# Kernel tuning notes

Measured on AMD Instinct MI355X. Metric: run time of the kernel, lower is better.

The kernel has to match this reference:

```python
import jax, jax.numpy as jnp
import numpy as np

B, N, E = 2, 4096, 768
H = 12
HD = E // H  # 64

def setup_inputs() -> dict:
    key = jax.random.key(0)
    k1, k2, k3, k4, k5 = jax.random.split(key, 5)
    s = 0.02
    return {
        "x": jax.random.normal(k1, (B, N, E), dtype=jnp.float32),
        "w_qkv": jax.random.normal(k2, (3 * E, E), dtype=jnp.float32) * s,
        "b_qkv": jax.random.normal(k3, (3 * E,), dtype=jnp.float32) * s,
        "w_proj": jax.random.normal(k4, (E, E), dtype=jnp.float32) * s,
        "b_proj": jax.random.normal(k5, (E,), dtype=jnp.float32) * s,
    }

def reference(x, w_qkv, b_qkv, w_proj, b_proj):
    b, n, e = x.shape
    hd = e // H
    # fused QKV projection (torch Linear: x @ W.T + b)
    qkv = jnp.einsum('bne,fe->bnf', x, w_qkv) + b_qkv          # [B,N,3E]
    # faithful to torch reshape(B,N,H,3*hd).permute(0,2,1,3).chunk(3,-1)
    qkv = qkv.reshape(b, n, H, 3 * hd).transpose(0, 2, 1, 3)    # [B,H,N,3hd]
    q, k, v = jnp.split(qkv, 3, axis=-1)                        # each [B,H,N,hd]
    attn = jnp.einsum('bhqd,bhkd->bhqk', q, k) / jnp.sqrt(jnp.float32(hd))
    attn = jax.nn.softmax(attn, axis=-1)                        # [B,H,N,N]
    # dropout layers are identity in eval mode
    out = jnp.einsum('bhqk,bhkd->bhqd', attn, v)                # [B,H,N,hd]
    out = out.transpose(0, 2, 1, 3).reshape(b, n, e)            # [B,N,E]
    out = jnp.einsum('bne,fe->bnf', out, w_proj) + b_proj
    return out
```

## Files before the change

### kernel.cpp

```cpp
#include <hip/hip_runtime.h>

typedef unsigned short u16;
typedef __bf16 bf16x8 __attribute__((ext_vector_type(8)));
typedef float f32x4 __attribute__((ext_vector_type(4)));
typedef unsigned short u16x8 __attribute__((ext_vector_type(8)));
typedef unsigned short u16x4 __attribute__((ext_vector_type(4)));

__device__ __forceinline__ u16 f2bf(float f) {
    __bf16 h = (__bf16)f;
    union { __bf16 h; u16 u; } cv; cv.h = h;
    return cv.u;
}

__device__ __forceinline__ f32x4 mfma16(bf16x8 a, bf16x8 b, f32x4 c) {
    return __builtin_amdgcn_mfma_f32_16x16x32_bf16(a, b, c, 0, 0, 0);
}

__device__ __forceinline__ void gll16(const u16* gp, u16* lp) {
    __builtin_amdgcn_global_load_lds(
        (__attribute__((address_space(1))) void*)const_cast<u16*>(gp),
        (__attribute__((address_space(3))) void*)lp,
        16, 0, 0);
}

__global__ __launch_bounds__(256) void cvt_bf16(const float* __restrict__ in,
                                                u16* __restrict__ out) {
    int i = blockIdx.x * 256 + threadIdx.x;
    const float4* p = (const float4*)in;
    float4 a = p[2 * i];
    float4 b = p[2 * i + 1];
    u16x8 r;
    r[0] = f2bf(a.x); r[1] = f2bf(a.y); r[2] = f2bf(a.z); r[3] = f2bf(a.w);
    r[4] = f2bf(b.x); r[5] = f2bf(b.y); r[6] = f2bf(b.z); r[7] = f2bf(b.w);
    *(u16x8*)&out[8 * i] = r;
}

__global__ __launch_bounds__(256) void gemm_qkv(
    const u16* __restrict__ A, const u16* __restrict__ W,
    const float* __restrict__ bias,
    u16* __restrict__ Qg, u16* __restrict__ Kg, u16* __restrict__ Vtg)
{
    __shared__ __attribute__((aligned(16))) u16 As[128 * 32];
    __shared__ __attribute__((aligned(16))) u16 Bs[128 * 32];
    const int tid = threadIdx.x;
    const int lane = tid & 63, wave = tid >> 6;
    const int lo = lane & 15, hi = lane >> 4;
    const int wm = (wave >> 1) * 64, wn = (wave & 1) * 64;
    const int m0 = blockIdx.y * 128, n0 = blockIdx.x * 128;

    f32x4 acc[4][4];
#pragma unroll
    for (int i = 0; i < 4; i++)
#pragma unroll
        for (int j = 0; j < 4; j++) acc[i][j] = f32x4{0.f, 0.f, 0.f, 0.f};

    const int ar = tid >> 2, ac = (tid & 3) * 8;
    const u16* ga = A + (size_t)(m0 + ar) * 768 + ac;
    const u16* gb = W + (size_t)(n0 + ar) * 768 + ac;

    for (int kt = 0; kt < 768; kt += 32) {
        gll16(ga + kt,            &As[tid * 8]);
        gll16(ga + kt + 64 * 768, &As[2048 + tid * 8]);
        gll16(gb + kt,            &Bs[tid * 8]);
        gll16(gb + kt + 64 * 768, &Bs[2048 + tid * 8]);
        __syncthreads();
        bf16x8 af[4], bfr[4];
#pragma unroll
        for (int mi = 0; mi < 4; mi++)
            af[mi] = *(const bf16x8*)&As[(wm + mi * 16 + lo) * 32 + hi * 8];
#pragma unroll
        for (int ni = 0; ni < 4; ni++)
            bfr[ni] = *(const bf16x8*)&Bs[(wn + ni * 16 + lo) * 32 + hi * 8];
#pragma unroll
        for (int mi = 0; mi < 4; mi++)
#pragma unroll
            for (int ni = 0; ni < 4; ni++)
                acc[mi][ni] = mfma16(af[mi], bfr[ni], acc[mi][ni]);
        __syncthreads();
    }

#pragma unroll
    for (int ni = 0; ni < 4; ni++) {
        const int n = n0 + wn + ni * 16 + lo;
        const int h = n / 192;
        const int rem = n - h * 192;
        const int sel = rem >> 6;
        const int d = rem & 63;
        const float bv = bias[n];
#pragma unroll
        for (int mi = 0; mi < 4; mi++) {
#pragma unroll
            for (int r = 0; r < 4; r++) {
                const int m = m0 + wm + mi * 16 + hi * 4 + r;
                const int bb = m >> 12;
                const int q = m & 4095;
                const float v = acc[mi][ni][r] + bv;
                const size_t bh = (size_t)(bb * 12 + h);
                if (sel == 0) {
                    Qg[(bh * 4096 + q) * 64 + d] = f2bf(v * 0.18033688011112042f);
                } else if (sel == 1) {
                    Kg[(bh * 4096 + q) * 64 + (d ^ ((q & 7) * 8))] = f2bf(v);
                } else {
                    Vtg[(bh * 64 + d) * 4096 +
                        ((q & ~63) | ((q & 63) ^ ((d & 7) * 8)))] = f2bf(v);
                }
            }
        }
    }
}

__global__ __launch_bounds__(256, 3) void attn_kernel(
    const u16* __restrict__ Qg, const u16* __restrict__ Kg,
    const u16* __restrict__ Vtg, u16* __restrict__ Ob)
{
    __shared__ __attribute__((aligned(16))) u16 Ks[128 * 64];
    __shared__ __attribute__((aligned(16))) u16 Vt[64 * 128];
    __shared__ __attribute__((aligned(16))) u16 Ps[8][16 * 64];
    const int tid = threadIdx.x;
    const int lane = tid & 63, wave = tid >> 6;
    const int lo = lane & 15, hi = lane >> 4;
    const int qt = blockIdx.x, h = blockIdx.y, b = blockIdx.z;
    const size_t bh = (size_t)(b * 12 + h);
    const int swl = (lo & 7) * 8;

    bf16x8 qf[2][2];
#pragma unroll
    for (int t = 0; t < 2; t++) {
        const int qrow = qt * 128 + wave * 32 + t * 16 + lo;
        const u16* qp = Qg + (bh * 4096 + qrow) * 64 + hi * 8;
        qf[t][0] = *(const bf16x8*)qp;
        qf[t][1] = *(const bf16x8*)(qp + 32);
    }
    f32x4 o[2][4];
#pragma unroll
    for (int t = 0; t < 2; t++)
#pragma unroll
        for (int i = 0; i < 4; i++) o[t][i] = f32x4{0.f, 0.f, 0.f, 0.f};
    float lp[2] = {0.f, 0.f};

    const u16* gk = Kg + (bh * 4096 + (tid >> 3)) * 64 + (tid & 7) * 8;
    const u16* gv = Vtg + (bh * 64 + (tid >> 4)) * 4096 + (tid & 15) * 8;

    for (int kt = 0; kt < 4096; kt += 128) {
#pragma unroll
        for (int c = 0; c < 4; c++)
            gll16(gk + (size_t)(kt + c * 32) * 64, &Ks[c * 2048 + tid * 8]);
#pragma unroll
        for (int c = 0; c < 4; c++)
            gll16(gv + kt + (size_t)c * 16 * 4096, &Vt[c * 2048 + tid * 8]);
        __syncthreads();

#pragma unroll
        for (int half = 0; half < 2; half++) {
            f32x4 st[2][4];
#pragma unroll
            for (int ni = 0; ni < 4; ni++) {
                const int row = half * 64 + ni * 16 + lo;
                const bf16x8 kf0 = *(const bf16x8*)&Ks[row * 64 + ((hi * 8) ^ swl)];
                const bf16x8 kf1 = *(const bf16x8*)&Ks[row * 64 + ((32 + hi * 8) ^ swl)];
                st[0][ni] = mfma16(kf0, qf[0][0], f32x4{0.f, 0.f, 0.f, 0.f});
                st[0][ni] = mfma16(kf1, qf[0][1], st[0][ni]);
                st[1][ni] = mfma16(kf0, qf[1][0], f32x4{0.f, 0.f, 0.f, 0.f});
                st[1][ni] = mfma16(kf1, qf[1][1], st[1][ni]);
            }
#pragma unroll
            for (int t = 0; t < 2; t++) {
#pragma unroll
                for (int ni = 0; ni < 4; ni++) {
                    u16x4 w;
#pragma unroll
                    for (int r = 0; r < 4; r++) {
                        const float p = __builtin_amdgcn_exp2f(st[t][ni][r]);
                        lp[t] += p;
                        w[r] = f2bf(p);
                    }
                    *(u16x4*)&Ps[wave * 2 + t]
                        [lo * 64 + ((ni * 16 + hi * 4) ^ swl)] = w;
                }
            }
            bf16x8 pf[2][2];
#pragma unroll
            for (int t = 0; t < 2; t++)
#pragma unroll
                for (int p = 0; p < 2; p++)
                    pf[t][p] = *(const bf16x8*)&Ps[wave * 2 + t]
                        [lo * 64 + ((p * 32 + hi * 8) ^ swl)];

#pragma unroll
            for (int di = 0; di < 4; di++) {
                const int base = (di * 16 + lo) * 128 + half * 64;
#pragma unroll
                for (int p = 0; p < 2; p++) {
                    const bf16x8 vt = *(const bf16x8*)
                        &Vt[base + ((p * 32 + hi * 8) ^ swl)];
                    o[0][di] = mfma16(pf[0][p], vt, o[0][di]);
                    o[1][di] = mfma16(pf[1][p], vt, o[1][di]);
                }
            }
        }
        __syncthreads();
    }

#pragma unroll
    for (int t = 0; t < 2; t++) {
        lp[t] += __shfl_xor(lp[t], 16, 64);
        lp[t] += __shfl_xor(lp[t], 32, 64);
    }

#pragma unroll
    for (int t = 0; t < 2; t++) {
#pragma unroll
        for (int r = 0; r < 4; r++) {
            const float rs = __shfl(lp[t], hi * 4 + r, 64);
            const float inv = 1.f / rs;
            const int q = qt * 128 + wave * 32 + t * 16 + hi * 4 + r;
            u16* op = Ob + ((size_t)b * 4096 + q) * 768 + h * 64 + lo;
#pragma unroll
            for (int di = 0; di < 4; di++)
                op[di * 16] = f2bf(o[t][di][r] * inv);
        }
    }
}

__global__ __launch_bounds__(256) void gemm_proj(
    const u16* __restrict__ A, const u16* __restrict__ W,
    const float* __restrict__ bias, float* __restrict__ C)
{
    __shared__ __attribute__((aligned(16))) u16 As[128 * 32];
    __shared__ __attribute__((aligned(16))) u16 Bs[128 * 32];
    const int tid = threadIdx.x;
    const int lane = tid & 63, wave = tid >> 6;
    const int lo = lane & 15, hi = lane >> 4;
    const int wm = (wave >> 1) * 64, wn = (wave & 1) * 64;
    const int m0 = blockIdx.y * 128, n0 = blockIdx.x * 128;

    f32x4 acc[4][4];
#pragma unroll
    for (int i = 0; i < 4; i++)
#pragma unroll
        for (int j = 0; j < 4; j++) acc[i][j] = f32x4{0.f, 0.f, 0.f, 0.f};

    const int ar = tid >> 2, ac = (tid & 3) * 8;
    const u16* ga = A + (size_t)(m0 + ar) * 768 + ac;
    const u16* gb = W + (size_t)(n0 + ar) * 768 + ac;

    for (int kt = 0; kt < 768; kt += 32) {
        gll16(ga + kt,            &As[tid * 8]);
        gll16(ga + kt + 64 * 768, &As[2048 + tid * 8]);
        gll16(gb + kt,            &Bs[tid * 8]);
        gll16(gb + kt + 64 * 768, &Bs[2048 + tid * 8]);
        __syncthreads();
        bf16x8 af[4], bfr[4];
#pragma unroll
        for (int mi = 0; mi < 4; mi++)
            af[mi] = *(const bf16x8*)&As[(wm + mi * 16 + lo) * 32 + hi * 8];
#pragma unroll
        for (int ni = 0; ni < 4; ni++)
            bfr[ni] = *(const bf16x8*)&Bs[(wn + ni * 16 + lo) * 32 + hi * 8];
#pragma unroll
        for (int mi = 0; mi < 4; mi++)
#pragma unroll
            for (int ni = 0; ni < 4; ni++)
                acc[mi][ni] = mfma16(af[mi], bfr[ni], acc[mi][ni]);
        __syncthreads();
    }

#pragma unroll
    for (int ni = 0; ni < 4; ni++) {
        const int n = n0 + wn + ni * 16 + lo;
        const float bv = bias[n];
#pragma unroll
        for (int mi = 0; mi < 4; mi++) {
#pragma unroll
            for (int r = 0; r < 4; r++) {
                const int m = m0 + wm + mi * 16 + hi * 4 + r;
                C[(size_t)m * 768 + n] = acc[mi][ni][r] + bv;
            }
        }
    }
}

extern "C" void kernel_launch(void* const* d_in, const int* in_sizes, int n_in,
                              void* d_out, int out_size, void* d_ws, size_t ws_size,
                              hipStream_t stream)
{
    const float* x      = (const float*)d_in[0];
    const float* w_qkv  = (const float*)d_in[1];
    const float* b_qkv  = (const float*)d_in[2];
    const float* w_proj = (const float*)d_in[3];
    const float* b_proj = (const float*)d_in[4];
    float* out = (float*)d_out;

    u16* ws  = (u16*)d_ws;
    u16* xb  = ws;
    u16* wqb = xb + 6291456;
    u16* wpb = wqb + 1769472;
    u16* Qg  = wpb + 589824;
    u16* Kg  = Qg + 6291456;
    u16* Vtg = Kg + 6291456;
    u16* Ob  = Vtg + 6291456;

    cvt_bf16<<<3072, 256, 0, stream>>>(x, xb);
    cvt_bf16<<<864,  256, 0, stream>>>(w_qkv, wqb);
    cvt_bf16<<<288,  256, 0, stream>>>(w_proj, wpb);
    gemm_qkv<<<dim3(18, 64), 256, 0, stream>>>(xb, wqb, b_qkv, Qg, Kg, Vtg);
    attn_kernel<<<dim3(32, 12, 2), 256, 0, stream>>>(Qg, Kg, Vtg, Ob);
    gemm_proj<<<dim3(6, 64), 256, 0, stream>>>(Ob, wpb, b_proj, out);
}
```

Baseline: 324.9 us.

## Use single-wave attention blocks loading K/V directly into registers

Attention is restructured so each block is one wave handling 64 query rows. K and V^T tiles are loaded straight from global memory into registers, with no LDS staging and no block barriers, and the swizzled K/V layouts written by the QKV GEMM are removed. The three conversion kernels are also merged into one launch to cut launch overhead. The risk is that K/V reuse across waves through LDS is lost, so global and L2 traffic rises. Register pressure also grows with four query tiles per wave.

```diff
diff --git a/kernel.cpp b/kernel.cpp
--- a/kernel.cpp
+++ b/kernel.cpp
@@ -23,16 +23,24 @@
         16, 0, 0);
 }
 
-__global__ __launch_bounds__(256) void cvt_bf16(const float* __restrict__ in,
-                                                u16* __restrict__ out) {
-    int i = blockIdx.x * 256 + threadIdx.x;
-    const float4* p = (const float4*)in;
+__global__ __launch_bounds__(256) void cvt_all(
+    const float* __restrict__ x, const float* __restrict__ wq,
+    const float* __restrict__ wp,
+    u16* __restrict__ xb, u16* __restrict__ wqb, u16* __restrict__ wpb)
+{
+    const int blk = blockIdx.x;
+    const float* src; u16* dst; int base;
+    if (blk < 3072)      { src = x;  dst = xb;  base = 0; }
+    else if (blk < 3936) { src = wq; dst = wqb; base = 3072; }
+    else                 { src = wp; dst = wpb; base = 3936; }
+    const int i = (blk - base) * 256 + threadIdx.x;
+    const float4* p = (const float4*)src;
     float4 a = p[2 * i];
     float4 b = p[2 * i + 1];
     u16x8 r;
     r[0] = f2bf(a.x); r[1] = f2bf(a.y); r[2] = f2bf(a.z); r[3] = f2bf(a.w);
     r[4] = f2bf(b.x); r[5] = f2bf(b.y); r[6] = f2bf(b.z); r[7] = f2bf(b.w);
-    *(u16x8*)&out[8 * i] = r;
+    *(u16x8*)&dst[8 * i] = r;
 }
 
 __global__ __launch_bounds__(256) void gemm_qkv(
@@ -99,121 +107,104 @@
                 if (sel == 0) {
                     Qg[(bh * 4096 + q) * 64 + d] = f2bf(v * 0.18033688011112042f);
                 } else if (sel == 1) {
-                    Kg[(bh * 4096 + q) * 64 + (d ^ ((q & 7) * 8))] = f2bf(v);
+                    Kg[(bh * 4096 + q) * 64 + d] = f2bf(v);
                 } else {
-                    Vtg[(bh * 64 + d) * 4096 +
-                        ((q & ~63) | ((q & 63) ^ ((d & 7) * 8)))] = f2bf(v);
+                    Vtg[(bh * 64 + d) * 4096 + q] = f2bf(v);
                 }
             }
         }
     }
 }
 
-__global__ __launch_bounds__(256, 3) void attn_kernel(
+__global__ __launch_bounds__(64, 2) void attn_kernel(
     const u16* __restrict__ Qg, const u16* __restrict__ Kg,
     const u16* __restrict__ Vtg, u16* __restrict__ Ob)
 {
-    __shared__ __attribute__((aligned(16))) u16 Ks[128 * 64];
-    __shared__ __attribute__((aligned(16))) u16 Vt[64 * 128];
-    __shared__ __attribute__((aligned(16))) u16 Ps[8][16 * 64];
-    const int tid = threadIdx.x;
-    const int lane = tid & 63, wave = tid >> 6;
+    __shared__ __attribute__((aligned(16))) u16 Ps[4][16 * 64];
+    const int lane = threadIdx.x & 63;
     const int lo = lane & 15, hi = lane >> 4;
-    const int qt = blockIdx.x, h = blockIdx.y, b = blockIdx.z;
+    const int qc = blockIdx.x, h = blockIdx.y, b = blockIdx.z;
     const size_t bh = (size_t)(b * 12 + h);
     const int swl = (lo & 7) * 8;
-
-    bf16x8 qf[2][2];
-#pragma unroll
-    for (int t = 0; t < 2; t++) {
-        const int qrow = qt * 128 + wave * 32 + t * 16 + lo;
-        const u16* qp = Qg + (bh * 4096 + qrow) * 64 + hi * 8;
+    const int qbase = qc * 64;
+
+    bf16x8 qf[4][2];
+#pragma unroll
+    for (int t = 0; t < 4; t++) {
+        const u16* qp = Qg + (bh * 4096 + qbase + t * 16 + lo) * 64 + hi * 8;
         qf[t][0] = *(const bf16x8*)qp;
         qf[t][1] = *(const bf16x8*)(qp + 32);
     }
-    f32x4 o[2][4];
-#pragma unroll
-    for (int t = 0; t < 2; t++)
+    f32x4 o[4][4];
+#pragma unroll
+    for (int t = 0; t < 4; t++)
 #pragma unroll
         for (int i = 0; i < 4; i++) o[t][i] = f32x4{0.f, 0.f, 0.f, 0.f};
-    float lp[2] = {0.f, 0.f};
-
-    const u16* gk = Kg + (bh * 4096 + (tid >> 3)) * 64 + (tid & 7) * 8;
-    const u16* gv = Vtg + (bh * 64 + (tid >> 4)) * 4096 + (tid & 15) * 8;
-
-    for (int kt = 0; kt < 4096; kt += 128) {
-#pragma unroll
-        for (int c = 0; c < 4; c++)
-            gll16(gk + (size_t)(kt + c * 32) * 64, &Ks[c * 2048 + tid * 8]);
-#pragma unroll
-        for (int c = 0; c < 4; c++)
-            gll16(gv + kt + (size_t)c * 16 * 4096, &Vt[c * 2048 + tid * 8]);
-        __syncthreads();
-
-#pragma unroll
-        for (int half = 0; half < 2; half++) {
-            f32x4 st[2][4];
+    float lp[4] = {0.f, 0.f, 0.f, 0.f};
+
+    const u16* Kb = Kg + bh * 4096 * 64;
+    const u16* Vb = Vtg + bh * 64 * 4096;
+
+    for (int kt = 0; kt < 4096; kt += 64) {
+        bf16x8 kf[4][2], vf[4][2];
+#pragma unroll
+        for (int ni = 0; ni < 4; ni++) {
+            const u16* kp = Kb + (size_t)(kt + ni * 16 + lo) * 64 + hi * 8;
+            kf[ni][0] = *(const bf16x8*)kp;
+            kf[ni][1] = *(const bf16x8*)(kp + 32);
+        }
+#pragma unroll
+        for (int di = 0; di < 4; di++) {
+            const u16* vp = Vb + (size_t)(di * 16 + lo) * 4096 + kt + hi * 8;
+            vf[di][0] = *(const bf16x8*)vp;
+            vf[di][1] = *(const bf16x8*)(vp + 32);
+        }
+
+#pragma unroll
+        for (int t = 0; t < 4; t++) {
+            f32x4 st[4];
 #pragma unroll
             for (int ni = 0; ni < 4; ni++) {
-                const int row = half * 64 + ni * 16 + lo;
-                const bf16x8 kf0 = *(const bf16x8*)&Ks[row * 64 + ((hi * 8) ^ swl)];
-                const bf16x8 kf1 = *(const bf16x8*)&Ks[row * 64 + ((32 + hi * 8) ^ swl)];
-                st[0][ni] = mfma16(kf0, qf[0][0], f32x4{0.f, 0.f, 0.f, 0.f});
-                st[0][ni] = mfma16(kf1, qf[0][1], st[0][ni]);
-                st[1][ni] = mfma16(kf0, qf[1][0], f32x4{0.f, 0.f, 0.f, 0.f});
-                st[1][ni] = mfma16(kf1, qf[1][1], st[1][ni]);
-            }
-#pragma unroll
-            for (int t = 0; t < 2; t++) {
-#pragma unroll
-                for (int ni = 0; ni < 4; ni++) {
-                    u16x4 w;
-#pragma unroll
-                    for (int r = 0; r < 4; r++) {
-                        const float p = __builtin_amdgcn_exp2f(st[t][ni][r]);
-                        lp[t] += p;
-                        w[r] = f2bf(p);
-                    }
-                    *(u16x4*)&Ps[wave * 2 + t]
-                        [lo * 64 + ((ni * 16 + hi * 4) ^ swl)] = w;
+                st[ni] = mfma16(kf[ni][0], qf[t][0], f32x4{0.f, 0.f, 0.f, 0.f});
+                st[ni] = mfma16(kf[ni][1], qf[t][1], st[ni]);
+            }
+#pragma unroll
+            for (int ni = 0; ni < 4; ni++) {
+                u16x4 w;
+#pragma unroll
+                for (int r = 0; r < 4; r++) {
+                    const float p = __builtin_amdgcn_exp2f(st[ni][r]);
+                    lp[t] += p;
+                    w[r] = f2bf(p);
                 }
-            }
-            bf16x8 pf[2][2];
-#pragma unroll
-            for (int t = 0; t < 2; t++)
-#pragma unroll
-                for (int p = 0; p < 2; p++)
-                    pf[t][p] = *(const bf16x8*)&Ps[wave * 2 + t]
-                        [lo * 64 + ((p * 32 + hi * 8) ^ swl)];
-
+                *(u16x4*)&Ps[t][lo * 64 + ((ni * 16 + hi * 4) ^ swl)] = w;
+            }
+        }
+#pragma unroll
+        for (int t = 0; t < 4; t++) {
+            bf16x8 pf0 = *(const bf16x8*)&Ps[t][lo * 64 + ((hi * 8) ^ swl)];
+            bf16x8 pf1 = *(const bf16x8*)&Ps[t][lo * 64 + ((32 + hi * 8) ^ swl)];
 #pragma unroll
             for (int di = 0; di < 4; di++) {
-                const int base = (di * 16 + lo) * 128 + half * 64;
-#pragma unroll
-                for (int p = 0; p < 2; p++) {
-                    const bf16x8 vt = *(const bf16x8*)
-                        &Vt[base + ((p * 32 + hi * 8) ^ swl)];
-                    o[0][di] = mfma16(pf[0][p], vt, o[0][di]);
-                    o[1][di] = mfma16(pf[1][p], vt, o[1][di]);
-                }
-            }
-        }
-        __syncthreads();
-    }
-
-#pragma unroll
-    for (int t = 0; t < 2; t++) {
+                o[t][di] = mfma16(pf0, vf[di][0], o[t][di]);
+                o[t][di] = mfma16(pf1, vf[di][1], o[t][di]);
+            }
+        }
+    }
+
+#pragma unroll
+    for (int t = 0; t < 4; t++) {
         lp[t] += __shfl_xor(lp[t], 16, 64);
         lp[t] += __shfl_xor(lp[t], 32, 64);
     }
 
 #pragma unroll
-    for (int t = 0; t < 2; t++) {
+    for (int t = 0; t < 4; t++) {
 #pragma unroll
         for (int r = 0; r < 4; r++) {
             const float rs = __shfl(lp[t], hi * 4 + r, 64);
             const float inv = 1.f / rs;
-            const int q = qt * 128 + wave * 32 + t * 16 + hi * 4 + r;
+            const int q = qbase + t * 16 + hi * 4 + r;
             u16* op = Ob + ((size_t)b * 4096 + q) * 768 + h * 64 + lo;
 #pragma unroll
             for (int di = 0; di < 4; di++)
@@ -300,10 +291,8 @@
     u16* Vtg = Kg + 6291456;
     u16* Ob  = Vtg + 6291456;
 
-    cvt_bf16<<<3072, 256, 0, stream>>>(x, xb);
-    cvt_bf16<<<864,  256, 0, stream>>>(w_qkv, wqb);
-    cvt_bf16<<<288,  256, 0, stream>>>(w_proj, wpb);
+    cvt_all<<<4224, 256, 0, stream>>>(x, w_qkv, w_proj, xb, wqb, wpb);
     gemm_qkv<<<dim3(18, 64), 256, 0, stream>>>(xb, wqb, b_qkv, Qg, Kg, Vtg);
-    attn_kernel<<<dim3(32, 12, 2), 256, 0, stream>>>(Qg, Kg, Vtg, Ob);
+    attn_kernel<<<dim3(64, 12, 2), 64, 0, stream>>>(Qg, Kg, Vtg, Ob);
     gemm_proj<<<dim3(6, 64), 256, 0, stream>>>(Ob, wpb, b_proj, out);
 }
```

Result: slower. 337.6 us (+3.9%).
